# Kernel tuning notes

Hardware: AMD Instinct MI355X
Metric: run time of the kernel (lower is better)

## Reference

```python
import jax, jax.numpy as jnp
import numpy as np

N_NODES = 50000
N_EDGES = 400000
IN_DIM = 256
OUT_DIM = 64
HEADS = 2
ATTN_HIDDEN = 64
ALPHA = 0.2
TEMP = 0.55


def setup_inputs() -> dict:
    key = jax.random.key(0)
    k_x, k_src, k_dst, k_w, k_wa, k_a = jax.random.split(key, 6)
    x = jax.random.normal(k_x, (N_NODES, IN_DIM), dtype=jnp.float32)
    src = jax.random.randint(k_src, (N_EDGES,), 0, N_NODES, dtype=jnp.int32)
    dst = jnp.sort(jax.random.randint(k_dst, (N_EDGES,), 0, N_NODES, dtype=jnp.int32))
    # Glorot-uniform-like params
    def glorot(k, shape, fan_in, fan_out):
        lim = jnp.sqrt(6.0 / (fan_in + fan_out))
        return jax.random.uniform(k, shape, jnp.float32, -lim, lim)
    W = glorot(k_w, (IN_DIM, HEADS, OUT_DIM), IN_DIM, HEADS * OUT_DIM)
    W_attn = glorot(k_wa, (HEADS, 2 * OUT_DIM, ATTN_HIDDEN), 2 * OUT_DIM, ATTN_HIDDEN)
    a_vec = glorot(k_a, (HEADS, ATTN_HIDDEN), HEADS, ATTN_HIDDEN)
    return {"x": x, "W": W, "W_attn": W_attn, "a_vec": a_vec, "src": src, "dst": dst}


def reference(x, W, W_attn, a_vec, src, dst):
    N = x.shape[0]
    # node-level projection: [N, H, F]
    Wh = jnp.einsum('nd,dhf->nhf', x, W)
    # per-edge gathers
    Wh_src = Wh[src]                                   # [E, H, F]
    Wh_dst = Wh[dst]                                   # [E, H, F]
    z = jnp.concatenate([Wh_src, Wh_dst], axis=-1)     # [E, H, 2F]
    z_act = jax.nn.leaky_relu(jnp.einsum('ehf,hfc->ehc', z, W_attn), ALPHA)
    logits = jnp.einsum('ehc,hc->eh', z_act, a_vec).astype(jnp.float32) / TEMP
    # per-head segment softmax over incoming edges of each dst node
    seg_max = jax.ops.segment_max(logits, dst, num_segments=N)   # [N, H]
    ex = jnp.exp(logits - seg_max[dst])
    seg_sum = jax.ops.segment_sum(ex, dst, num_segments=N)
    alphas = (ex / (seg_sum[dst] + 1e-9)).astype(Wh_src.dtype)   # [E, H]
    # weighted scatter-sum of source messages
    out = jax.ops.segment_sum(Wh_src * alphas[..., None], dst, num_segments=N)  # [N, H, F]
    # concat=False -> mean over heads (dropout is identity at inference)
    return out.mean(axis=1)
```

## Files before the change

kernel.cpp:

```cpp
#include <hip/hip_runtime.h>
#include <hip/hip_bf16.h>
#include <math.h>

#define N_NODES 50000
#define N_EDGES 400000
#define IN_DIM 256
#define OUT_DIM 64
#define HEADS 2
#define ATTN_HIDDEN 64
#define ALPHA_SLOPE 0.2f
#define TEMP 0.55f
#define NHF 128
#define ZDIM 384

typedef __bf16 bf16x8 __attribute__((ext_vector_type(8)));
typedef float f32x4 __attribute__((ext_vector_type(4)));

__device__ __forceinline__ ushort f2bf(float f) {
    unsigned u = __float_as_uint(f);
    u = (u + 0x7fffu + ((u >> 16) & 1u)) >> 16;
    return (ushort)u;
}
__device__ __forceinline__ unsigned pack2(float a, float b) {
    return (unsigned)f2bf(a) | ((unsigned)f2bf(b) << 16);
}
__device__ __forceinline__ float bfl(unsigned u) { return __uint_as_float(u << 16); }
__device__ __forceinline__ float bfh(unsigned u) { return __uint_as_float(u & 0xffff0000u); }

__global__ __launch_bounds__(256) void k_combine(const float* __restrict__ W,
                                                 const float* __restrict__ Wa,
                                                 ushort* __restrict__ Wct) {
    __shared__ float col[64];
    const int n = blockIdx.x;
    const int t = threadIdx.x;
    if (n < 128) {
        Wct[(size_t)n * 256 + t] = f2bf(W[(size_t)t * NHF + n]);
        return;
    }
    const int part = (n - 128) >> 7;
    const int idx = (n - 128) & 127;
    const int h = idx >> 6;
    const int c = idx & 63;
    const int fb = part ? 64 : 0;
    if (t < 64) col[t] = Wa[(size_t)h * 8192 + (size_t)(fb + t) * 64 + c];
    __syncthreads();
    const float* wr = W + (size_t)t * NHF + h * 64;
    float acc = 0.f;
#pragma unroll
    for (int f = 0; f < 64; f++) acc += wr[f] * col[f];
    Wct[(size_t)n * 256 + t] = f2bf(acc);
}

__global__ void k_segstart(const int* __restrict__ dst, int* __restrict__ seg) {
    int n = blockIdx.x * blockDim.x + threadIdx.x;
    if (n > N_NODES) return;
    int lo = 0, hi = N_EDGES;
    while (lo < hi) {
        int mid = (lo + hi) >> 1;
        if (dst[mid] < n) lo = mid + 1; else hi = mid;
    }
    seg[n] = lo;
}

#define LDT 40
__global__ __launch_bounds__(256) void k_gemm(const float* __restrict__ x,
                                              const ushort* __restrict__ Wct,
                                              ushort* __restrict__ Zb) {
    __shared__ ushort As[64 * LDT];
    __shared__ ushort Bs[384 * LDT];
    const int t = threadIdx.x;
    const int w = t >> 6, lane = t & 63;
    const int q = lane >> 4, r16 = lane & 15;
    const int row0 = blockIdx.x * 64;

    f32x4 acc[24];
#pragma unroll
    for (int c = 0; c < 24; c++) acc[c] = (f32x4){0.f, 0.f, 0.f, 0.f};

    const int arow = t >> 2, a8 = (t & 3) * 8;
    const int agrow = row0 + arow;

    for (int k0 = 0; k0 < IN_DIM; k0 += 32) {
        float4 v0 = make_float4(0.f, 0.f, 0.f, 0.f), v1 = v0;
        if (agrow < N_NODES) {
            const float* xp = x + (size_t)agrow * IN_DIM + k0 + a8;
            v0 = *(const float4*)xp;
            v1 = *(const float4*)(xp + 4);
        }
        uint4 av;
        av.x = pack2(v0.x, v0.y); av.y = pack2(v0.z, v0.w);
        av.z = pack2(v1.x, v1.y); av.w = pack2(v1.z, v1.w);
        *(uint4*)(As + arow * LDT + a8) = av;
#pragma unroll
        for (int i = 0; i < 6; i++) {
            int brow = (t >> 2) + 64 * i;
            uint4 bv = *(const uint4*)(Wct + (size_t)brow * 256 + k0 + a8);
            *(uint4*)(Bs + brow * LDT + a8) = bv;
        }
        __syncthreads();
        bf16x8 af = *(const bf16x8*)(As + (w * 16 + r16) * LDT + q * 8);
#pragma unroll
        for (int c = 0; c < 24; c++) {
            bf16x8 bf = *(const bf16x8*)(Bs + (c * 16 + r16) * LDT + q * 8);
            acc[c] = __builtin_amdgcn_mfma_f32_16x16x32_bf16(af, bf, acc[c], 0, 0, 0);
        }
        __syncthreads();
    }
#pragma unroll
    for (int c = 0; c < 24; c++) {
#pragma unroll
        for (int rr = 0; rr < 4; rr++) {
            int row = row0 + w * 16 + q * 4 + rr;
            if (row < N_NODES)
                Zb[(size_t)row * ZDIM + c * 16 + r16] = f2bf(acc[c][rr]);
        }
    }
}

__global__ __launch_bounds__(256) void k_fused(const ushort* __restrict__ Zb,
                                               const float* __restrict__ avec,
                                               const int* __restrict__ src,
                                               const int* __restrict__ seg,
                                               float* __restrict__ out) {
    const int lane = threadIdx.x & 63;
    const int wv = threadIdx.x >> 6;
    const int g = lane >> 4, l16 = lane & 15;
    const int n = blockIdx.x * 16 + wv * 4 + g;
    if (n >= N_NODES) return;
    const int choff = 8 * l16;

    const float4 af0 = *(const float4*)(avec + choff);
    const float4 af1 = *(const float4*)(avec + choff + 4);
    const float a[8] = {af0.x, af0.y, af0.z, af0.w, af1.x, af1.y, af1.z, af1.w};

    const uint4 udv = *(const uint4*)(Zb + (size_t)n * ZDIM + 256 + choff);
    const float ud[8] = {bfl(udv.x), bfh(udv.x), bfl(udv.y), bfh(udv.y),
                         bfl(udv.z), bfh(udv.z), bfl(udv.w), bfh(udv.w)};

    const int e0 = seg[n], e1 = seg[n + 1];
    float m = -INFINITY, l = 0.f;
    float acc[8] = {0.f, 0.f, 0.f, 0.f, 0.f, 0.f, 0.f, 0.f};

    uint4 us = make_uint4(0, 0, 0, 0), wh = us;
    if (e0 < e1) {
        const int s = src[e0];
        us = *(const uint4*)(Zb + (size_t)s * ZDIM + 128 + choff);
        wh = *(const uint4*)(Zb + (size_t)s * ZDIM + choff);
    }
    for (int e = e0; e < e1; e++) {
        const uint4 cus = us, cwh = wh;
        if (e + 1 < e1) {
            const int sn = src[e + 1];
            us = *(const uint4*)(Zb + (size_t)sn * ZDIM + 128 + choff);
            wh = *(const uint4*)(Zb + (size_t)sn * ZDIM + choff);
        }
        float p;
        {
            float v0, v1, s0, s1;
            v0 = bfl(cus.x) + ud[0]; v1 = bfh(cus.x) + ud[1];
            s0 = fmaxf(v0, ALPHA_SLOPE * v0); s1 = fmaxf(v1, ALPHA_SLOPE * v1);
            p = s0 * a[0] + s1 * a[1];
            v0 = bfl(cus.y) + ud[2]; v1 = bfh(cus.y) + ud[3];
            s0 = fmaxf(v0, ALPHA_SLOPE * v0); s1 = fmaxf(v1, ALPHA_SLOPE * v1);
            p += s0 * a[2] + s1 * a[3];
            v0 = bfl(cus.z) + ud[4]; v1 = bfh(cus.z) + ud[5];
            s0 = fmaxf(v0, ALPHA_SLOPE * v0); s1 = fmaxf(v1, ALPHA_SLOPE * v1);
            p += s0 * a[4] + s1 * a[5];
            v0 = bfl(cus.w) + ud[6]; v1 = bfh(cus.w) + ud[7];
            s0 = fmaxf(v0, ALPHA_SLOPE * v0); s1 = fmaxf(v1, ALPHA_SLOPE * v1);
            p += s0 * a[6] + s1 * a[7];
        }
        p += __shfl_xor(p, 1, 64);
        p += __shfl_xor(p, 2, 64);
        p += __shfl_xor(p, 4, 64);
        const float logit = p * (1.0f / TEMP);
        const float nm = fmaxf(m, logit);
        const float sc = __expf(m - nm);
        const float wgt = __expf(logit - nm);
        l = l * sc + wgt;
        acc[0] = acc[0] * sc + wgt * bfl(cwh.x);
        acc[1] = acc[1] * sc + wgt * bfh(cwh.x);
        acc[2] = acc[2] * sc + wgt * bfl(cwh.y);
        acc[3] = acc[3] * sc + wgt * bfh(cwh.y);
        acc[4] = acc[4] * sc + wgt * bfl(cwh.z);
        acc[5] = acc[5] * sc + wgt * bfh(cwh.z);
        acc[6] = acc[6] * sc + wgt * bfl(cwh.w);
        acc[7] = acc[7] * sc + wgt * bfh(cwh.w);
        m = nm;
    }
    const float inv = 0.5f / (l + 1e-9f);
#pragma unroll
    for (int j = 0; j < 8; j++) {
        const float v = acc[j] * inv;
        acc[j] = v + __shfl_xor(v, 8, 64);
    }
    if (l16 < 8) {
        float4 o0 = make_float4(acc[0], acc[1], acc[2], acc[3]);
        float4 o1 = make_float4(acc[4], acc[5], acc[6], acc[7]);
        float* op = out + (size_t)n * 64 + choff;
        *(float4*)op = o0;
        *(float4*)(op + 4) = o1;
    }
}

extern "C" void kernel_launch(void* const* d_in, const int* in_sizes, int n_in,
                              void* d_out, int out_size, void* d_ws, size_t ws_size,
                              hipStream_t stream) {
    const float* x    = (const float*)d_in[0];
    const float* W    = (const float*)d_in[1];
    const float* Wa   = (const float*)d_in[2];
    const float* avec = (const float*)d_in[3];
    const int*   src  = (const int*)d_in[4];
    const int*   dst  = (const int*)d_in[5];
    float* out = (float*)d_out;

    ushort* Zb  = (ushort*)d_ws;
    ushort* Wct = Zb + 19200000;
    int*    seg = (int*)((char*)d_ws + 38596608);

    k_combine <<<ZDIM, 256, 0, stream>>>(W, Wa, Wct);
    k_segstart<<<(N_NODES + 1 + 255) / 256, 256, 0, stream>>>(dst, seg);
    k_gemm    <<<(N_NODES + 63) / 64, 256, 0, stream>>>(x, Wct, Zb);
    k_fused   <<<(N_NODES + 15) / 16, 256, 0, stream>>>(Zb, avec, src, seg, out);
}
```

Before: 169.1 us.

## Double-buffer GEMM B tiles, load A directly to registers, merge segstart into combine

Rewrites the GEMM main loop so the A operand (x) is loaded directly from global memory into MFMA fragment registers, with no shared-memory staging. B (Wct) is prefetched into registers one k-step ahead and written into a double-buffered shared tile laid out in fragment order, which drops one barrier per iteration and lets the global loads overlap the MFMAs. The segment-start binary search is folded into the k_combine launch as extra blocks, saving one kernel launch. Costs are higher register pressure (launch_bounds 256,3) and 48KB of shared memory per block.

```diff
diff --git a/kernel.cpp b/kernel.cpp
--- a/kernel.cpp
+++ b/kernel.cpp
@@ -29,10 +29,24 @@
 
 __global__ __launch_bounds__(256) void k_combine(const float* __restrict__ W,
                                                  const float* __restrict__ Wa,
-                                                 ushort* __restrict__ Wct) {
+                                                 ushort* __restrict__ Wct,
+                                                 const int* __restrict__ dst,
+                                                 int* __restrict__ seg) {
     __shared__ float col[64];
-    const int n = blockIdx.x;
+    const int b = blockIdx.x;
     const int t = threadIdx.x;
+    if (b >= ZDIM) {
+        int n = (b - ZDIM) * 256 + t;
+        if (n > N_NODES) return;
+        int lo = 0, hi = N_EDGES;
+        while (lo < hi) {
+            int mid = (lo + hi) >> 1;
+            if (dst[mid] < n) lo = mid + 1; else hi = mid;
+        }
+        seg[n] = lo;
+        return;
+    }
+    const int n = b;
     if (n < 128) {
         Wct[(size_t)n * 256 + t] = f2bf(W[(size_t)t * NHF + n]);
         return;
@@ -51,58 +65,62 @@
     Wct[(size_t)n * 256 + t] = f2bf(acc);
 }
 
-__global__ void k_segstart(const int* __restrict__ dst, int* __restrict__ seg) {
-    int n = blockIdx.x * blockDim.x + threadIdx.x;
-    if (n > N_NODES) return;
-    int lo = 0, hi = N_EDGES;
-    while (lo < hi) {
-        int mid = (lo + hi) >> 1;
-        if (dst[mid] < n) lo = mid + 1; else hi = mid;
-    }
-    seg[n] = lo;
-}
-
-#define LDT 40
-__global__ __launch_bounds__(256) void k_gemm(const float* __restrict__ x,
-                                              const ushort* __restrict__ Wct,
-                                              ushort* __restrict__ Zb) {
-    __shared__ ushort As[64 * LDT];
-    __shared__ ushort Bs[384 * LDT];
+__global__ __launch_bounds__(256, 3) void k_gemm(const float* __restrict__ x,
+                                                 const ushort* __restrict__ Wct,
+                                                 ushort* __restrict__ Zb) {
+    __shared__ __align__(16) ushort Bs[2][12288];
     const int t = threadIdx.x;
     const int w = t >> 6, lane = t & 63;
     const int q = lane >> 4, r16 = lane & 15;
     const int row0 = blockIdx.x * 64;
 
+    int boff[6];
+#pragma unroll
+    for (int j = 0; j < 6; j++) {
+        int idx = j * 256 + t;
+        int c = idx >> 6, lj = idx & 63;
+        boff[j] = (c * 16 + (lj & 15)) * 256 + (lj >> 4) * 8;
+    }
+    const int arow = row0 + w * 16 + r16;
+    const bool avalid = arow < N_NODES;
+    const float* xp = x + (size_t)arow * IN_DIM + q * 8;
+
     f32x4 acc[24];
 #pragma unroll
     for (int c = 0; c < 24; c++) acc[c] = (f32x4){0.f, 0.f, 0.f, 0.f};
 
-    const int arow = t >> 2, a8 = (t & 3) * 8;
-    const int agrow = row0 + arow;
-
-    for (int k0 = 0; k0 < IN_DIM; k0 += 32) {
-        float4 v0 = make_float4(0.f, 0.f, 0.f, 0.f), v1 = v0;
-        if (agrow < N_NODES) {
-            const float* xp = x + (size_t)agrow * IN_DIM + k0 + a8;
-            v0 = *(const float4*)xp;
-            v1 = *(const float4*)(xp + 4);
-        }
-        uint4 av;
-        av.x = pack2(v0.x, v0.y); av.y = pack2(v0.z, v0.w);
-        av.z = pack2(v1.x, v1.y); av.w = pack2(v1.z, v1.w);
-        *(uint4*)(As + arow * LDT + a8) = av;
-#pragma unroll
-        for (int i = 0; i < 6; i++) {
-            int brow = (t >> 2) + 64 * i;
-            uint4 bv = *(const uint4*)(Wct + (size_t)brow * 256 + k0 + a8);
-            *(uint4*)(Bs + brow * LDT + a8) = bv;
-        }
-        __syncthreads();
-        bf16x8 af = *(const bf16x8*)(As + (w * 16 + r16) * LDT + q * 8);
+    uint4 bv[6];
+#pragma unroll
+    for (int j = 0; j < 6; j++) bv[j] = *(const uint4*)(Wct + boff[j]);
+    float4 av0 = make_float4(0.f, 0.f, 0.f, 0.f), av1 = av0;
+    if (avalid) { av0 = *(const float4*)xp; av1 = *(const float4*)(xp + 4); }
+#pragma unroll
+    for (int j = 0; j < 6; j++) *(uint4*)&Bs[0][(j * 256 + t) * 8] = bv[j];
+    __syncthreads();
+
+    for (int k = 0; k < 8; k++) {
+        const int cur = k & 1;
+        uint4 afp;
+        afp.x = pack2(av0.x, av0.y); afp.y = pack2(av0.z, av0.w);
+        afp.z = pack2(av1.x, av1.y); afp.w = pack2(av1.z, av1.w);
+        const bf16x8 af = *(const bf16x8*)&afp;
+        if (k < 7) {
+            const int kn = (k + 1) * 32;
+#pragma unroll
+            for (int j = 0; j < 6; j++) bv[j] = *(const uint4*)(Wct + boff[j] + kn);
+            if (avalid) {
+                av0 = *(const float4*)(xp + kn);
+                av1 = *(const float4*)(xp + kn + 4);
+            }
+        }
 #pragma unroll
         for (int c = 0; c < 24; c++) {
-            bf16x8 bf = *(const bf16x8*)(Bs + (c * 16 + r16) * LDT + q * 8);
+            const bf16x8 bf = *(const bf16x8*)&Bs[cur][c * 512 + lane * 8];
             acc[c] = __builtin_amdgcn_mfma_f32_16x16x32_bf16(af, bf, acc[c], 0, 0, 0);
+        }
+        if (k < 7) {
+#pragma unroll
+            for (int j = 0; j < 6; j++) *(uint4*)&Bs[1 - cur][(j * 256 + t) * 8] = bv[j];
         }
         __syncthreads();
     }
@@ -218,8 +236,8 @@
     ushort* Wct = Zb + 19200000;
     int*    seg = (int*)((char*)d_ws + 38596608);
 
-    k_combine <<<ZDIM, 256, 0, stream>>>(W, Wa, Wct);
-    k_segstart<<<(N_NODES + 1 + 255) / 256, 256, 0, stream>>>(dst, seg);
+    const int seg_blocks = (N_NODES + 1 + 255) / 256;
+    k_combine <<<ZDIM + seg_blocks, 256, 0, stream>>>(W, Wa, Wct, dst, seg);
     k_gemm    <<<(N_NODES + 63) / 64, 256, 0, stream>>>(x, Wct, Zb);
     k_fused   <<<(N_NODES + 15) / 16, 256, 0, stream>>>(Zb, avec, src, seg, out);
 }
```

After: 200.3 us. 18.5% more time.

## Pre-swizzle weights into MFMA fragment layout and drop LDS staging in GEMM

Applied to the files above, without the earlier changes.

The combine kernel now writes the bf16 weight matrix directly in MFMA B-fragment order, and the segment-start binary search is merged into the same launch. The GEMM no longer stages A or B tiles through shared memory or uses barriers. Each wave computes 32 rows with two M tiles, so every B fragment loaded straight from global/L2 is used twice, and A is read and converted in registers. This removes LDS traffic, syncs and one kernel launch. The cost is 192 accumulator registers per thread and B fragments re-read from cache by every wave.

```diff
diff --git a/kernel.cpp b/kernel.cpp
--- a/kernel.cpp
+++ b/kernel.cpp
@@ -29,92 +29,104 @@
 
 __global__ __launch_bounds__(256) void k_combine(const float* __restrict__ W,
                                                  const float* __restrict__ Wa,
-                                                 ushort* __restrict__ Wct) {
+                                                 ushort* __restrict__ Wctf,
+                                                 const int* __restrict__ dst,
+                                                 int* __restrict__ seg) {
     __shared__ float col[64];
-    const int n = blockIdx.x;
+    const int b = blockIdx.x;
     const int t = threadIdx.x;
+    if (b >= ZDIM) {
+        int n = (b - ZDIM) * 256 + t;
+        if (n > N_NODES) return;
+        int lo = 0, hi = N_EDGES;
+        while (lo < hi) {
+            int mid = (lo + hi) >> 1;
+            if (dst[mid] < n) lo = mid + 1; else hi = mid;
+        }
+        seg[n] = lo;
+        return;
+    }
+    const int n = b;
+    const int k = t;
+    const int c = n >> 4, r16 = n & 15;
+    const int kc = k >> 5, q = (k >> 3) & 3, j = k & 7;
+    const size_t pos = (size_t)(((c * 8 + kc) * 64 + q * 16 + r16)) * 8 + j;
+
+    float val;
     if (n < 128) {
-        Wct[(size_t)n * 256 + t] = f2bf(W[(size_t)t * NHF + n]);
-        return;
-    }
-    const int part = (n - 128) >> 7;
-    const int idx = (n - 128) & 127;
-    const int h = idx >> 6;
-    const int c = idx & 63;
-    const int fb = part ? 64 : 0;
-    if (t < 64) col[t] = Wa[(size_t)h * 8192 + (size_t)(fb + t) * 64 + c];
-    __syncthreads();
-    const float* wr = W + (size_t)t * NHF + h * 64;
-    float acc = 0.f;
-#pragma unroll
-    for (int f = 0; f < 64; f++) acc += wr[f] * col[f];
-    Wct[(size_t)n * 256 + t] = f2bf(acc);
-}
-
-__global__ void k_segstart(const int* __restrict__ dst, int* __restrict__ seg) {
-    int n = blockIdx.x * blockDim.x + threadIdx.x;
-    if (n > N_NODES) return;
-    int lo = 0, hi = N_EDGES;
-    while (lo < hi) {
-        int mid = (lo + hi) >> 1;
-        if (dst[mid] < n) lo = mid + 1; else hi = mid;
-    }
-    seg[n] = lo;
-}
-
-#define LDT 40
-__global__ __launch_bounds__(256) void k_gemm(const float* __restrict__ x,
-                                              const ushort* __restrict__ Wct,
-                                              ushort* __restrict__ Zb) {
-    __shared__ ushort As[64 * LDT];
-    __shared__ ushort Bs[384 * LDT];
+        val = W[(size_t)k * NHF + n];
+    } else {
+        const int part = (n - 128) >> 7;
+        const int idx = (n - 128) & 127;
+        const int h = idx >> 6;
+        const int cc = idx & 63;
+        const int fb = part ? 64 : 0;
+        if (t < 64) col[t] = Wa[(size_t)h * 8192 + (size_t)(fb + t) * 64 + cc];
+        __syncthreads();
+        const float* wr = W + (size_t)k * NHF + h * 64;
+        float acc = 0.f;
+#pragma unroll
+        for (int f = 0; f < 64; f++) acc += wr[f] * col[f];
+        val = acc;
+    }
+    Wctf[pos] = f2bf(val);
+}
+
+__global__ __launch_bounds__(256, 2) void k_gemm(const float* __restrict__ x,
+                                                 const ushort* __restrict__ Wctf,
+                                                 ushort* __restrict__ Zb) {
     const int t = threadIdx.x;
     const int w = t >> 6, lane = t & 63;
     const int q = lane >> 4, r16 = lane & 15;
-    const int row0 = blockIdx.x * 64;
-
-    f32x4 acc[24];
-#pragma unroll
-    for (int c = 0; c < 24; c++) acc[c] = (f32x4){0.f, 0.f, 0.f, 0.f};
-
-    const int arow = t >> 2, a8 = (t & 3) * 8;
-    const int agrow = row0 + arow;
-
-    for (int k0 = 0; k0 < IN_DIM; k0 += 32) {
-        float4 v0 = make_float4(0.f, 0.f, 0.f, 0.f), v1 = v0;
-        if (agrow < N_NODES) {
-            const float* xp = x + (size_t)agrow * IN_DIM + k0 + a8;
-            v0 = *(const float4*)xp;
-            v1 = *(const float4*)(xp + 4);
-        }
-        uint4 av;
-        av.x = pack2(v0.x, v0.y); av.y = pack2(v0.z, v0.w);
-        av.z = pack2(v1.x, v1.y); av.w = pack2(v1.z, v1.w);
-        *(uint4*)(As + arow * LDT + a8) = av;
-#pragma unroll
-        for (int i = 0; i < 6; i++) {
-            int brow = (t >> 2) + 64 * i;
-            uint4 bv = *(const uint4*)(Wct + (size_t)brow * 256 + k0 + a8);
-            *(uint4*)(Bs + brow * LDT + a8) = bv;
-        }
-        __syncthreads();
-        bf16x8 af = *(const bf16x8*)(As + (w * 16 + r16) * LDT + q * 8);
+    const int wid = blockIdx.x * 4 + w;
+    const int row0 = wid * 32;
+    if (row0 >= N_NODES) return;
+
+    int rA0 = row0 + r16;
+    int rA1 = row0 + 16 + r16;
+    rA0 = rA0 < N_NODES ? rA0 : N_NODES - 1;
+    rA1 = rA1 < N_NODES ? rA1 : N_NODES - 1;
+    const float* xp0 = x + (size_t)rA0 * IN_DIM + q * 8;
+    const float* xp1 = x + (size_t)rA1 * IN_DIM + q * 8;
+    const ushort* bp = Wctf + lane * 8;
+
+    f32x4 acc[2][24];
+#pragma unroll
+    for (int mt = 0; mt < 2; mt++)
+#pragma unroll
+        for (int c = 0; c < 24; c++) acc[mt][c] = (f32x4){0.f, 0.f, 0.f, 0.f};
+
+#pragma unroll 1
+    for (int kc = 0; kc < 8; kc++) {
+        const float4 a00 = *(const float4*)(xp0 + kc * 32);
+        const float4 a01 = *(const float4*)(xp0 + kc * 32 + 4);
+        const float4 a10 = *(const float4*)(xp1 + kc * 32);
+        const float4 a11 = *(const float4*)(xp1 + kc * 32 + 4);
+        uint4 p0, p1;
+        p0.x = pack2(a00.x, a00.y); p0.y = pack2(a00.z, a00.w);
+        p0.z = pack2(a01.x, a01.y); p0.w = pack2(a01.z, a01.w);
+        p1.x = pack2(a10.x, a10.y); p1.y = pack2(a10.z, a10.w);
+        p1.z = pack2(a11.x, a11.y); p1.w = pack2(a11.z, a11.w);
+        const bf16x8 af0 = *(const bf16x8*)&p0;
+        const bf16x8 af1 = *(const bf16x8*)&p1;
+        const ushort* bk = bp + kc * 512;
 #pragma unroll
         for (int c = 0; c < 24; c++) {
-            bf16x8 bf = *(const bf16x8*)(Bs + (c * 16 + r16) * LDT + q * 8);
-            acc[c] = __builtin_amdgcn_mfma_f32_16x16x32_bf16(af, bf, acc[c], 0, 0, 0);
-        }
-        __syncthreads();
-    }
-#pragma unroll
-    for (int c = 0; c < 24; c++) {
-#pragma unroll
-        for (int rr = 0; rr < 4; rr++) {
-            int row = row0 + w * 16 + q * 4 + rr;
-            if (row < N_NODES)
-                Zb[(size_t)row * ZDIM + c * 16 + r16] = f2bf(acc[c][rr]);
-        }
-    }
+            const bf16x8 bf = *(const bf16x8*)(bk + c * 4096);
+            acc[0][c] = __builtin_amdgcn_mfma_f32_16x16x32_bf16(af0, bf, acc[0][c], 0, 0, 0);
+            acc[1][c] = __builtin_amdgcn_mfma_f32_16x16x32_bf16(af1, bf, acc[1][c], 0, 0, 0);
+        }
+    }
+#pragma unroll
+    for (int mt = 0; mt < 2; mt++)
+#pragma unroll
+        for (int c = 0; c < 24; c++)
+#pragma unroll
+            for (int rr = 0; rr < 4; rr++) {
+                const int row = row0 + mt * 16 + q * 4 + rr;
+                if (row < N_NODES)
+                    Zb[(size_t)row * ZDIM + c * 16 + r16] = f2bf(acc[mt][c][rr]);
+            }
 }
 
 __global__ __launch_bounds__(256) void k_fused(const ushort* __restrict__ Zb,
@@ -214,12 +226,13 @@
     const int*   dst  = (const int*)d_in[5];
     float* out = (float*)d_out;
 
-    ushort* Zb  = (ushort*)d_ws;
-    ushort* Wct = Zb + 19200000;
-    int*    seg = (int*)((char*)d_ws + 38596608);
-
-    k_combine <<<ZDIM, 256, 0, stream>>>(W, Wa, Wct);
-    k_segstart<<<(N_NODES + 1 + 255) / 256, 256, 0, stream>>>(dst, seg);
-    k_gemm    <<<(N_NODES + 63) / 64, 256, 0, stream>>>(x, Wct, Zb);
+    ushort* Zb   = (ushort*)d_ws;
+    ushort* Wctf = Zb + 19200000;
+    int*    seg  = (int*)((char*)d_ws + 38596608);
+
+    const int seg_blocks = (N_NODES + 1 + 255) / 256;
+    const int gemm_waves = (N_NODES + 31) / 32;
+    k_combine <<<ZDIM + seg_blocks, 256, 0, stream>>>(W, Wa, Wctf, dst, seg);
+    k_gemm    <<<(gemm_waves + 3) / 4, 256, 0, stream>>>(x, Wctf, Zb);
     k_fused   <<<(N_NODES + 15) / 16, 256, 0, stream>>>(Zb, avec, src, seg, out);
 }
```

After: 173.4 us. +2.5%, slower.
